# Optimization experiments

Hardware: AMD Instinct MI355X
Metric: run time of the kernel (lower is better)

The kernel has to match this reference:

```python
import jax, jax.numpy as jnp
import numpy as np

B, L = 4, 256          # batch, tokens per example
V = 100000             # conceptnet_len (vocab)
E = 256                # emb_size (== da for self-attention)


def setup_inputs() -> dict:
    key = jax.random.key(0)
    k1, k2, k3 = jax.random.split(key, 3)
    conceptnet_text_vec = jax.random.randint(k1, (B, L), 0, V, dtype=jnp.int64)
    # Embedding table and self-attention params (xavier-ish scale)
    table = jax.random.normal(k2, (V, E), dtype=jnp.float32) * (1.0 / np.sqrt(E))
    ka, kb = jax.random.split(k3)
    a = jax.random.normal(ka, (E, E), dtype=jnp.float32) * np.sqrt(2.0 / (E + E)) * 1.414
    b = jax.random.normal(kb, (E, 1), dtype=jnp.float32) * np.sqrt(2.0 / (E + 1)) * 1.414
    return {"conceptnet_text_vec": conceptnet_text_vec, "table": table, "a": a, "b": b, "topk": 16}


def reference(conceptnet_text_vec, table, a, b, topk):
    # emb: [B, L, E] gather from table
    emb = table[conceptnet_text_vec]
    # dense similarity against full table: [B, L, V]
    logits = jnp.einsum("ble,ve->blv", emb, table)
    match = jax.nn.softmax(logits, axis=-1)
    # top-k neighbor indices: [B, L, K]
    _, idx = jax.lax.top_k(match, topk)
    # second gather: [B, L, K, E]
    h = table[idx]
    # self-attention pool over the K retrieved concepts
    # e: [B, L, 1, K]
    e = jnp.swapaxes(jnp.matmul(jnp.tanh(jnp.matmul(h, a)), b), -1, -2)
    attention = jax.nn.softmax(e, axis=-1)
    # [B, L, 1, E] -> [B, L, E]
    att_emb = jnp.matmul(attention, h).squeeze(-2)
    return att_emb
```

## Files before the change

kernel.cpp:

```cpp
#include <hip/hip_runtime.h>


#define V_ROWS   100000
#define E_DIM    256
#define M_TOK    1024
#define NGROUPS  98
#define VGROUP   1024
#define NCAND    (NGROUPS*8)
#define KBIAS    2.5f

typedef _Float16 f16x8 __attribute__((ext_vector_type(8)));
typedef float    f32x4 __attribute__((ext_vector_type(4)));

__global__ __launch_bounds__(256) void prep_kernel(
    const float* __restrict__ table, const int* __restrict__ text,
    const float* __restrict__ amat,
    _Float16* __restrict__ tabh, _Float16* __restrict__ embh,
    _Float16* __restrict__ ahT)
{
  const int NTAB = V_ROWS * E_DIM / 8;
  const int NEMB = M_TOK * E_DIM / 8;
  const int NA   = E_DIM * E_DIM;
  const int NU   = NTAB + NEMB + NA;
  for (int u = blockIdx.x * 256 + threadIdx.x; u < NU; u += gridDim.x * 256) {
    if (u < NTAB + NEMB) {
      size_t srcoff; _Float16* dst;
      if (u < NTAB) {
        srcoff = (size_t)u * 8; dst = tabh + (size_t)u * 8;
      } else {
        int e2 = u - NTAB; int tt = e2 >> 5, kc = e2 & 31;
        srcoff = (size_t)text[tt] * E_DIM + kc * 8;
        dst = embh + (size_t)e2 * 8;
      }
      float4 x0 = *(const float4*)(table + srcoff);
      float4 x1 = *(const float4*)(table + srcoff + 4);
      f16x8 hv;
      hv[0]=(_Float16)x0.x; hv[1]=(_Float16)x0.y; hv[2]=(_Float16)x0.z; hv[3]=(_Float16)x0.w;
      hv[4]=(_Float16)x1.x; hv[5]=(_Float16)x1.y; hv[6]=(_Float16)x1.z; hv[7]=(_Float16)x1.w;
      *(f16x8*)dst = hv;
    } else {
      int e3 = u - NTAB - NEMB;
      int k = e3 >> 8, n = e3 & 255;
      ahT[n * E_DIM + k] = (_Float16)amat[e3];
    }
  }
}

__device__ __forceinline__ unsigned int pack_key(float val, int lidx) {
  float b = val + KBIAS;
  unsigned int u = __builtin_bit_cast(unsigned int, b);
  return (((u >> 7) & 0xFFFFu) << 10) | (unsigned int)lidx;
}
__device__ __forceinline__ float thr_from_key(unsigned int key) {
  unsigned int u = 0x40000000u | ((key >> 10) << 7);
  return __builtin_bit_cast(float, u) - KBIAS;
}

__global__ __launch_bounds__(256)
__attribute__((amdgpu_waves_per_eu(2, 3)))
void gemm_topk_kernel(
    const _Float16* __restrict__ tabh, const _Float16* __restrict__ embh,
    unsigned int* __restrict__ cand)
{
  int bid = blockIdx.x;
  int group, mtile;
  if (bid < 1536) { int xcd = bid & 7, r = bid >> 3; mtile = r & 15; group = xcd * 12 + (r >> 4); }
  else            { int r = bid - 1536;              mtile = r & 15; group = 96 + (r >> 4); }

  const int tid = threadIdx.x;
  const int w = tid >> 6, l = tid & 63;

  __shared__ uint4 Alds[64 * 32];
  __shared__ uint4 Cl[64 * 17];

  {
    const uint4* srcA = (const uint4*)embh + (size_t)mtile * 64 * 32;
    #pragma unroll
    for (int i = 0; i < 8; ++i) {
      int c = i * 256 + tid;
      int r = c >> 5, kc = c & 31;
      Alds[r * 32 + (kc ^ (r & 7))] = srcA[c];
    }
  }
  __syncthreads();

  const int limit = (group == NGROUPS - 1) ? (V_ROWS - (NGROUPS - 1) * VGROUP) : VGROUP;
  unsigned int t4[4][4] = {{0,0,0,0},{0,0,0,0},{0,0,0,0},{0,0,0,0}};
  float thr[4] = {-0.5f, -0.5f, -0.5f, -0.5f};

  const int rbase = group * VGROUP + w * 64 + (l & 15);
  const int koff  = (l >> 4) * 8;

  f16x8 bufA[4], bufB[4];

#define LOADB(BUF, G, KK)                                                    \
  {                                                                          \
    _Pragma("unroll")                                                        \
    for (int fv = 0; fv < 4; ++fv) {                                         \
      int v = rbase + (G) * 256 + fv * 16;                                   \
      v = v < V_ROWS ? v : V_ROWS - 1;                                       \
      BUF[fv] = *reinterpret_cast<const f16x8*>(                             \
          tabh + ((size_t)v << 8) + (KK) * 32 + koff);                       \
    }                                                                        \
  }

  LOADB(bufA, 0, 0)
  LOADB(bufB, 0, 1)

  f32x4 acc[4][4];

#define KSTEP(G, KK, BUF, DOPRE, PG, PKK)                                    \
  {                                                                          \
    int cs = ((KK) * 4 + (l >> 4)) ^ (l & 7);                                \
    f16x8 af0 = *reinterpret_cast<const f16x8*>(&Alds[((l & 15)      ) * 32 + cs]); \
    f16x8 af1 = *reinterpret_cast<const f16x8*>(&Alds[(16 + (l & 15)) * 32 + cs]);  \
    f16x8 af2 = *reinterpret_cast<const f16x8*>(&Alds[(32 + (l & 15)) * 32 + cs]);  \
    f16x8 af3 = *reinterpret_cast<const f16x8*>(&Alds[(48 + (l & 15)) * 32 + cs]);  \
    _Pragma("unroll")                                                        \
    for (int fv = 0; fv < 4; ++fv) {                                         \
      acc[fv][0] = __builtin_amdgcn_mfma_f32_16x16x32_f16(BUF[fv], af0, acc[fv][0], 0, 0, 0); \
      acc[fv][1] = __builtin_amdgcn_mfma_f32_16x16x32_f16(BUF[fv], af1, acc[fv][1], 0, 0, 0); \
      acc[fv][2] = __builtin_amdgcn_mfma_f32_16x16x32_f16(BUF[fv], af2, acc[fv][2], 0, 0, 0); \
      acc[fv][3] = __builtin_amdgcn_mfma_f32_16x16x32_f16(BUF[fv], af3, acc[fv][3], 0, 0, 0); \
    }                                                                        \
    if (DOPRE) LOADB(BUF, PG, PKK)                                           \
  }

  for (int g = 0; g < 4; ++g) {
    #pragma unroll
    for (int fv = 0; fv < 4; ++fv)
      #pragma unroll
      for (int fm = 0; fm < 4; ++fm)
        acc[fv][fm] = (f32x4){0.f, 0.f, 0.f, 0.f};

    KSTEP(g, 0, bufA, 1, g, 2)
    KSTEP(g, 1, bufB, 1, g, 3)
    KSTEP(g, 2, bufA, 1, g, 4)
    KSTEP(g, 3, bufB, 1, g, 5)
    KSTEP(g, 4, bufA, 1, g, 6)
    KSTEP(g, 5, bufB, 1, g, 7)
    KSTEP(g, 6, bufA, (g < 3), g + 1, 0)
    KSTEP(g, 7, bufB, (g < 3), g + 1, 1)

    int qb = g * 256 + w * 64 + ((l >> 4) << 2);
    #pragma unroll
    for (int fv = 0; fv < 4; ++fv) {
      int lb = qb + fv * 16;
      if (lb + 4 <= limit) {
        #pragma unroll
        for (int fm = 0; fm < 4; ++fm) {
          f32x4 v = acc[fv][fm];
          float m = fmaxf(fmaxf(v[0], v[1]), fmaxf(v[2], v[3]));
          if (m > thr[fm]) {
            #pragma unroll
            for (int e = 0; e < 4; ++e) {
              if (v[e] > thr[fm]) {
                unsigned int kx = pack_key(v[e], lb + e);
                #pragma unroll
                for (int q = 0; q < 4; ++q) {
                  unsigned int mx = t4[fm][q] > kx ? t4[fm][q] : kx;
                  unsigned int mn = t4[fm][q] > kx ? kx : t4[fm][q];
                  t4[fm][q] = mx; kx = mn;
                }
                thr[fm] = thr_from_key(t4[fm][3]);
              }
            }
          }
        }
      }
    }
  }
#undef KSTEP
#undef LOADB

  #pragma unroll
  for (int fm = 0; fm < 4; ++fm) {
    int token = fm * 16 + (l & 15);
    int contrib = w * 4 + (l >> 4);
    Cl[token * 17 + contrib] = make_uint4(t4[fm][0], t4[fm][1], t4[fm][2], t4[fm][3]);
  }
  __syncthreads();
  if (tid < 64) {
    unsigned int best[8] = {0,0,0,0,0,0,0,0};
    #pragma unroll 4
    for (int c = 0; c < 16; ++c) {
      uint4 q4 = Cl[tid * 17 + c];
      unsigned int ks[4] = {q4.x, q4.y, q4.z, q4.w};
      #pragma unroll
      for (int e = 0; e < 4; ++e) {
        unsigned int kx = ks[e];
        if (kx > best[7]) {
          #pragma unroll
          for (int q = 0; q < 8; ++q) {
            unsigned int mx = best[q] > kx ? best[q] : kx;
            unsigned int mn = best[q] > kx ? kx : best[q];
            best[q] = mx; kx = mn;
          }
        }
      }
    }
    unsigned int* dst = cand + ((size_t)(mtile * 64 + tid) * NGROUPS + group) * 8;
    #pragma unroll
    for (int i = 0; i < 8; ++i) dst[i] = best[i];
  }
}

__global__ __launch_bounds__(256) void select_kernel(
    const float* __restrict__ table, const int* __restrict__ text,
    const unsigned int* __restrict__ cand, int* __restrict__ hidx)
{
  const int t = blockIdx.x, tid = threadIdx.x;
  const int lane = tid & 63, w = tid >> 6;
  __shared__ unsigned int ck[NCAND];
  __shared__ unsigned long long pool[NCAND];
  __shared__ int hist[64];
  __shared__ int selv[32];
  __shared__ float ex[32];
  __shared__ int sh_b, sh_above, sh_c1, sh_c2;

  if (tid < 64) hist[tid] = 0;
  if (tid == 0) { sh_c1 = 0; sh_c2 = 0; }
  __syncthreads();

  for (int i = tid; i < NCAND; i += 256) {
    unsigned int k = cand[(size_t)t * NCAND + i];
    ck[i] = k;
    atomicAdd(&hist[k >> 20], 1);
  }
  __syncthreads();

  if (w == 0) {
    int v = hist[lane];
    int u;
    u = __shfl_down(v, 1);  if (lane < 63) v += u;
    u = __shfl_down(v, 2);  if (lane < 62) v += u;
    u = __shfl_down(v, 4);  if (lane < 60) v += u;
    u = __shfl_down(v, 8);  if (lane < 56) v += u;
    u = __shfl_down(v, 16); if (lane < 48) v += u;
    u = __shfl_down(v, 32); if (lane < 32) v += u;
    unsigned long long msk = __ballot(v >= 32);
    int b = 63 - __builtin_clzll(msk);
    int above = (b < 63) ? __shfl(v, b + 1) : 0;
    if (lane == 0) { sh_b = b; sh_above = above; }
  }
  __syncthreads();

  const int b = sh_b;
  for (int i = tid; i < NCAND; i += 256) {
    unsigned int k = ck[i];
    unsigned int bk = k >> 20;
    if (bk > (unsigned)b) {
      int p = atomicAdd(&sh_c1, 1);
      selv[p] = (i >> 3) * VGROUP + (int)(k & 1023u);
    } else if (bk == (unsigned)b) {
      int p = atomicAdd(&sh_c2, 1);
      pool[p] = ((unsigned long long)k << 20) | ((unsigned long long)i << 10)
              | (unsigned long long)p;
    }
  }
  __syncthreads();

  const int C = sh_above, R = 32 - C;
  if (w == 0) {
    int n2 = sh_c2;
    for (int it = 0; it < R; ++it) {
      unsigned long long best = 0;
      for (int i = lane; i < n2; i += 64) {
        unsigned long long p = pool[i];
        if (p > best) best = p;
      }
      #pragma unroll
      for (int d = 32; d >= 1; d >>= 1) {
        unsigned long long o = __shfl_xor(best, d);
        if (o > best) best = o;
      }
      if (lane == 0) {
        int pos  = (int)(best & 1023ull);
        int slot = (int)((best >> 10) & 1023ull);
        unsigned int k = (unsigned int)(best >> 20);
        selv[C + it] = (slot >> 3) * VGROUP + (int)(k & 1023u);
        pool[pos] = 0;
      }
    }
  }
  __syncthreads();

  {
    int c = tid >> 3, s = tid & 7;
    int tok = text[t];
    const float* er = table + (size_t)tok * E_DIM;
    const float* tr = table + (size_t)selv[c] * E_DIM;
    float acc = 0.f;
    #pragma unroll 8
    for (int k2 = 0; k2 < 32; ++k2) acc += er[s * 32 + k2] * tr[s * 32 + k2];
    #pragma unroll
    for (int d = 1; d < 8; d <<= 1) acc += __shfl_xor(acc, d);
    if (s == 0) ex[c] = acc;
  }
  __syncthreads();

  if (w == 0) {
    float val = (lane < 32) ? ex[lane] : -1e38f;
    for (int it = 0; it < 16; ++it) {
      float m = val;
      #pragma unroll
      for (int d = 1; d < 32; d <<= 1) { float o = __shfl_xor(m, d); m = o > m ? o : m; }
      unsigned long long msk = __ballot(lane < 32 && val == m);
      int winner = __ffsll(msk) - 1;
      if (lane == 0) hidx[t * 16 + it] = selv[winner];
      if (lane == winner) val = -1e38f;
    }
  }
}

__global__ __launch_bounds__(256) void gemm_attn_kernel(
    const _Float16* __restrict__ tabh, const _Float16* __restrict__ ahT,
    const float* __restrict__ table, const float* __restrict__ bvec,
    const int* __restrict__ hidx, float* __restrict__ out)
{
  const int mtile = blockIdx.x;
  const int tid = threadIdx.x;
  const int w = tid >> 6, l = tid & 63;
  __shared__ uint4 Alds[64 * 32];
  __shared__ int   hx[64];
  __shared__ float ep[64][5];
  __shared__ float wg[64];

  if (tid < 64) hx[tid] = hidx[mtile * 64 + tid];
  __syncthreads();

  #pragma unroll
  for (int i = 0; i < 8; ++i) {
    int c = i * 256 + tid;
    int r = c >> 5, kc = c & 31;
    Alds[r * 32 + (kc ^ (r & 7))] =
        *(const uint4*)(tabh + ((size_t)hx[r] << 8) + kc * 8);
  }
  __syncthreads();

  f32x4 acc[4][4];
  #pragma unroll
  for (int fm = 0; fm < 4; ++fm)
    #pragma unroll
    for (int fn = 0; fn < 4; ++fn)
      acc[fm][fn] = (f32x4){0.f, 0.f, 0.f, 0.f};

  #pragma unroll
  for (int kk = 0; kk < 8; ++kk) {
    int cs = (kk * 4 + (l >> 4)) ^ (l & 7);
    f16x8 af[4], bf[4];
    #pragma unroll
    for (int fm = 0; fm < 4; ++fm)
      af[fm] = *reinterpret_cast<const f16x8*>(&Alds[(fm * 16 + (l & 15)) * 32 + cs]);
    #pragma unroll
    for (int fn = 0; fn < 4; ++fn)
      bf[fn] = *reinterpret_cast<const f16x8*>(
          ahT + (size_t)(w * 64 + fn * 16 + (l & 15)) * E_DIM + kk * 32 + (l >> 4) * 8);
    #pragma unroll
    for (int fm = 0; fm < 4; ++fm)
      #pragma unroll
      for (int fn = 0; fn < 4; ++fn)
        acc[fm][fn] = __builtin_amdgcn_mfma_f32_16x16x32_f16(af[fm], bf[fn], acc[fm][fn], 0, 0, 0);
  }

  float bv[4];
  #pragma unroll
  for (int fn = 0; fn < 4; ++fn) bv[fn] = bvec[w * 64 + fn * 16 + (l & 15)];

  #pragma unroll
  for (int fm = 0; fm < 4; ++fm) {
    #pragma unroll
    for (int r2 = 0; r2 < 4; ++r2) {
      float s = tanhf(acc[fm][0][r2]) * bv[0] + tanhf(acc[fm][1][r2]) * bv[1]
              + tanhf(acc[fm][2][r2]) * bv[2] + tanhf(acc[fm][3][r2]) * bv[3];
      s += __shfl_xor(s, 1); s += __shfl_xor(s, 2);
      s += __shfl_xor(s, 4); s += __shfl_xor(s, 8);
      if ((l & 15) == 0) ep[fm * 16 + (l >> 4) * 4 + r2][w] = s;
    }
  }
  __syncthreads();

  if (tid < 64) {
    float e = ep[tid][0] + ep[tid][1] + ep[tid][2] + ep[tid][3];
    float m = e;
    m = fmaxf(m, __shfl_xor(m, 1)); m = fmaxf(m, __shfl_xor(m, 2));
    m = fmaxf(m, __shfl_xor(m, 4)); m = fmaxf(m, __shfl_xor(m, 8));
    float p = expf(e - m);
    float ssum = p;
    ssum += __shfl_xor(ssum, 1); ssum += __shfl_xor(ssum, 2);
    ssum += __shfl_xor(ssum, 4); ssum += __shfl_xor(ssum, 8);
    wg[tid] = p / ssum;
  }
  __syncthreads();

  {
    int token = w;
    int c4 = l * 4;
    float4 o = make_float4(0.f, 0.f, 0.f, 0.f);
    #pragma unroll
    for (int i = 0; i < 16; ++i) {
      float wt = wg[token * 16 + i];
      float4 h = *(const float4*)(table + ((size_t)hx[token * 16 + i] << 8) + c4);
      o.x += wt * h.x; o.y += wt * h.y; o.z += wt * h.z; o.w += wt * h.w;
    }
    *(float4*)(out + (size_t)(mtile * 4 + token) * E_DIM + c4) = o;
  }
}

extern "C" void kernel_launch(void* const* d_in, const int* in_sizes, int n_in,
                              void* d_out, int out_size, void* d_ws, size_t ws_size,
                              hipStream_t stream) {
  const int*   text  = (const int*)d_in[0];
  const float* table = (const float*)d_in[1];
  const float* amat  = (const float*)d_in[2];
  const float* bvec  = (const float*)d_in[3];
  float*       out   = (float*)d_out;

  char* ws = (char*)d_ws;
  _Float16*     tabh = (_Float16*)(ws + 0);
  _Float16*     embh = (_Float16*)(ws + 51200000);
  _Float16*     ahT  = (_Float16*)(ws + 51724288);
  unsigned int* cand = (unsigned int*)(ws + 51855360);
  int*          hidx = (int*)(ws + 55066624);

  prep_kernel<<<2048, 256, 0, stream>>>(table, text, amat, tabh, embh, ahT);
  gemm_topk_kernel<<<16 * NGROUPS, 256, 0, stream>>>(tabh, embh, cand);
  select_kernel<<<M_TOK, 256, 0, stream>>>(table, text, cand, hidx);
  gemm_attn_kernel<<<256, 256, 0, stream>>>(tabh, ahT, table, bvec, hidx, out);
}
```

Baseline: 387.6 us.

## Halve per-wave accumulator tile and alias LDS buffers to raise occupancy

The GEMM+topk kernel now processes each 256-row group in two halves of 32 rows per wave instead of 64. This halves the accumulator and B-fragment register footprint, and the waves_per_eu hint is raised from (2,3) to (3,4). The candidate-merge LDS buffer now reuses the A-tile storage, with an added barrier, to cut shared memory per block. The trade-off is that each A fragment read from LDS now feeds half as many MFMAs, so LDS reads per MFMA double and the inner loop has more iterations, in exchange for more waves to hide global-load latency.

```diff
diff --git a/kernel.cpp b/kernel.cpp
--- a/kernel.cpp
+++ b/kernel.cpp
@@ -57,7 +57,7 @@
 }
 
 __global__ __launch_bounds__(256)
-__attribute__((amdgpu_waves_per_eu(2, 3)))
+__attribute__((amdgpu_waves_per_eu(3, 4)))
 void gemm_topk_kernel(
     const _Float16* __restrict__ tabh, const _Float16* __restrict__ embh,
     unsigned int* __restrict__ cand)
@@ -70,8 +70,8 @@
   const int tid = threadIdx.x;
   const int w = tid >> 6, l = tid & 63;
 
-  __shared__ uint4 Alds[64 * 32];
-  __shared__ uint4 Cl[64 * 17];
+  __shared__ uint4 Slds[64 * 32];
+  uint4* Alds = Slds;
 
   {
     const uint4* srcA = (const uint4*)embh + (size_t)mtile * 64 * 32;
@@ -91,25 +91,21 @@
   const int rbase = group * VGROUP + w * 64 + (l & 15);
   const int koff  = (l >> 4) * 8;
 
-  f16x8 bufA[4], bufB[4];
-
-#define LOADB(BUF, G, KK)                                                    \
+  f16x8 bufA[2], bufB[2];
+  f32x4 acc[2][4];
+
+#define LOADB(BUF, G, HH, KK)                                                \
   {                                                                          \
     _Pragma("unroll")                                                        \
-    for (int fv = 0; fv < 4; ++fv) {                                         \
-      int v = rbase + (G) * 256 + fv * 16;                                   \
+    for (int fv2 = 0; fv2 < 2; ++fv2) {                                      \
+      int v = rbase + (G) * 256 + ((HH) * 2 + fv2) * 16;                     \
       v = v < V_ROWS ? v : V_ROWS - 1;                                       \
-      BUF[fv] = *reinterpret_cast<const f16x8*>(                             \
+      BUF[fv2] = *reinterpret_cast<const f16x8*>(                            \
           tabh + ((size_t)v << 8) + (KK) * 32 + koff);                       \
     }                                                                        \
   }
 
-  LOADB(bufA, 0, 0)
-  LOADB(bufB, 0, 1)
-
-  f32x4 acc[4][4];
-
-#define KSTEP(G, KK, BUF, DOPRE, PG, PKK)                                    \
+#define KSTEP(KK, BUF, DOPRE, PG, PHH, PKK)                                  \
   {                                                                          \
     int cs = ((KK) * 4 + (l >> 4)) ^ (l & 7);                                \
     f16x8 af0 = *reinterpret_cast<const f16x8*>(&Alds[((l & 15)      ) * 32 + cs]); \
@@ -117,52 +113,61 @@
     f16x8 af2 = *reinterpret_cast<const f16x8*>(&Alds[(32 + (l & 15)) * 32 + cs]);  \
     f16x8 af3 = *reinterpret_cast<const f16x8*>(&Alds[(48 + (l & 15)) * 32 + cs]);  \
     _Pragma("unroll")                                                        \
-    for (int fv = 0; fv < 4; ++fv) {                                         \
-      acc[fv][0] = __builtin_amdgcn_mfma_f32_16x16x32_f16(BUF[fv], af0, acc[fv][0], 0, 0, 0); \
-      acc[fv][1] = __builtin_amdgcn_mfma_f32_16x16x32_f16(BUF[fv], af1, acc[fv][1], 0, 0, 0); \
-      acc[fv][2] = __builtin_amdgcn_mfma_f32_16x16x32_f16(BUF[fv], af2, acc[fv][2], 0, 0, 0); \
-      acc[fv][3] = __builtin_amdgcn_mfma_f32_16x16x32_f16(BUF[fv], af3, acc[fv][3], 0, 0, 0); \
+    for (int fv2 = 0; fv2 < 2; ++fv2) {                                      \
+      acc[fv2][0] = __builtin_amdgcn_mfma_f32_16x16x32_f16(BUF[fv2], af0, acc[fv2][0], 0, 0, 0); \
+      acc[fv2][1] = __builtin_amdgcn_mfma_f32_16x16x32_f16(BUF[fv2], af1, acc[fv2][1], 0, 0, 0); \
+      acc[fv2][2] = __builtin_amdgcn_mfma_f32_16x16x32_f16(BUF[fv2], af2, acc[fv2][2], 0, 0, 0); \
+      acc[fv2][3] = __builtin_amdgcn_mfma_f32_16x16x32_f16(BUF[fv2], af3, acc[fv2][3], 0, 0, 0); \
     }                                                                        \
-    if (DOPRE) LOADB(BUF, PG, PKK)                                           \
-  }
+    if (DOPRE) LOADB(BUF, PG, PHH, PKK)                                      \
+  }
+
+  LOADB(bufA, 0, 0, 0)
+  LOADB(bufB, 0, 0, 1)
 
   for (int g = 0; g < 4; ++g) {
-    #pragma unroll
-    for (int fv = 0; fv < 4; ++fv)
-      #pragma unroll
-      for (int fm = 0; fm < 4; ++fm)
-        acc[fv][fm] = (f32x4){0.f, 0.f, 0.f, 0.f};
-
-    KSTEP(g, 0, bufA, 1, g, 2)
-    KSTEP(g, 1, bufB, 1, g, 3)
-    KSTEP(g, 2, bufA, 1, g, 4)
-    KSTEP(g, 3, bufB, 1, g, 5)
-    KSTEP(g, 4, bufA, 1, g, 6)
-    KSTEP(g, 5, bufB, 1, g, 7)
-    KSTEP(g, 6, bufA, (g < 3), g + 1, 0)
-    KSTEP(g, 7, bufB, (g < 3), g + 1, 1)
-
-    int qb = g * 256 + w * 64 + ((l >> 4) << 2);
-    #pragma unroll
-    for (int fv = 0; fv < 4; ++fv) {
-      int lb = qb + fv * 16;
-      if (lb + 4 <= limit) {
+    for (int hh = 0; hh < 2; ++hh) {
+      #pragma unroll
+      for (int fv2 = 0; fv2 < 2; ++fv2)
         #pragma unroll
-        for (int fm = 0; fm < 4; ++fm) {
-          f32x4 v = acc[fv][fm];
-          float m = fmaxf(fmaxf(v[0], v[1]), fmaxf(v[2], v[3]));
-          if (m > thr[fm]) {
-            #pragma unroll
-            for (int e = 0; e < 4; ++e) {
-              if (v[e] > thr[fm]) {
-                unsigned int kx = pack_key(v[e], lb + e);
-                #pragma unroll
-                for (int q = 0; q < 4; ++q) {
-                  unsigned int mx = t4[fm][q] > kx ? t4[fm][q] : kx;
-                  unsigned int mn = t4[fm][q] > kx ? kx : t4[fm][q];
-                  t4[fm][q] = mx; kx = mn;
+        for (int fm = 0; fm < 4; ++fm)
+          acc[fv2][fm] = (f32x4){0.f, 0.f, 0.f, 0.f};
+
+      const int ng  = (hh == 0) ? g : g + 1;
+      const int nhh = (hh == 0) ? 1 : 0;
+      const int last = (g == 3) && (hh == 1);
+
+      KSTEP(0, bufA, 1, g, hh, 2)
+      KSTEP(1, bufB, 1, g, hh, 3)
+      KSTEP(2, bufA, 1, g, hh, 4)
+      KSTEP(3, bufB, 1, g, hh, 5)
+      KSTEP(4, bufA, 1, g, hh, 6)
+      KSTEP(5, bufB, 1, g, hh, 7)
+      KSTEP(6, bufA, (!last), ng, nhh, 0)
+      KSTEP(7, bufB, (!last), ng, nhh, 1)
+
+      int qb = g * 256 + w * 64 + ((l >> 4) << 2);
+      #pragma unroll
+      for (int fv2 = 0; fv2 < 2; ++fv2) {
+        int lb = qb + (hh * 2 + fv2) * 16;
+        if (lb + 4 <= limit) {
+          #pragma unroll
+          for (int fm = 0; fm < 4; ++fm) {
+            f32x4 v = acc[fv2][fm];
+            float m = fmaxf(fmaxf(v[0], v[1]), fmaxf(v[2], v[3]));
+            if (m > thr[fm]) {
+              #pragma unroll
+              for (int e = 0; e < 4; ++e) {
+                if (v[e] > thr[fm]) {
+                  unsigned int kx = pack_key(v[e], lb + e);
+                  #pragma unroll
+                  for (int q = 0; q < 4; ++q) {
+                    unsigned int mx = t4[fm][q] > kx ? t4[fm][q] : kx;
+                    unsigned int mn = t4[fm][q] > kx ? kx : t4[fm][q];
+                    t4[fm][q] = mx; kx = mn;
+                  }
+                  thr[fm] = thr_from_key(t4[fm][3]);
                 }
-                thr[fm] = thr_from_key(t4[fm][3]);
               }
             }
           }
@@ -173,6 +178,8 @@
 #undef KSTEP
 #undef LOADB
 
+  __syncthreads();
+  uint4* Cl = Slds;
   #pragma unroll
   for (int fm = 0; fm < 4; ++fm) {
     int token = fm * 16 + (l & 15);
```

Result: slower. 433.9 us (+12.0%).
